# Performance work log

Measured on AMD Instinct MI355X. Metric: run time of the kernel, lower is better.

Reference implementation:

```python
import jax, jax.numpy as jnp
import numpy as np

N = 8192       # node_num
F_IN = 256     # src_feature
F_OUT = 128    # out_feature
NEG_SLOPE = 0.2  # standard GAT leakyrelu slope
MASK_VAL = -1e12


def setup_inputs() -> dict:
    key = jax.random.key(0)
    k1, k2, k3, k4, k5, k6 = jax.random.split(key, 6)
    x = jax.random.normal(k1, (N, F_IN), dtype=jnp.float32)
    adj = jax.random.randint(k2, (N, N), 0, 2, dtype=jnp.int32)  # 0/1 adjacency mask
    # xavier-uniform-like scales
    W = jax.random.normal(k3, (F_IN, F_OUT), dtype=jnp.float32) * np.float32(1.0 / np.sqrt(F_IN))
    a1 = jax.random.normal(k4, (F_OUT,), dtype=jnp.float32) * np.float32(0.1)  # att[:F_OUT]
    a2 = jax.random.normal(k5, (F_OUT,), dtype=jnp.float32) * np.float32(0.1)  # att[F_OUT:]
    bias = jax.random.normal(k6, (F_OUT,), dtype=jnp.float32) * np.float32(0.1)
    return {"x": x, "adj": adj, "W": W, "a1": a1, "a2": a2, "bias": bias}


def reference(x, adj, W, a1, a2, bias):
    # h = x @ W1  (src_h == dst_h for int src_dst_feature)
    h = x @ W  # [N, F_OUT]
    # e[i,j] = leakyrelu(att^T [h_i || h_j]) decomposed as (h@a1)_i + (h@a2)_j
    s_src = h @ a1  # [N]
    s_dst = h @ a2  # [N]
    e = jax.nn.leaky_relu(s_src[:, None] + s_dst[None, :], NEG_SLOPE)  # [N, N]
    masked = jnp.where(adj > 0, e, jnp.float32(MASK_VAL))
    attention = jax.nn.softmax(masked, axis=1)  # [N, N]
    # dropout in eval mode = identity; aggregate neighbor features
    out = attention @ h + bias  # [N, F_OUT]
    return out
```

## Files before the change

kernel.cpp:

```cpp
#include <hip/hip_runtime.h>
#include <cstdint>
#include <cstddef>

#define NN 8192
#define FIN 256
#define FOUT 128
#define SLOPE 0.2f
#define SHIFT 8.0f

typedef float f32x4 __attribute__((ext_vector_type(4)));
typedef __bf16 bf16x8 __attribute__((ext_vector_type(8)));
typedef int i32x4 __attribute__((ext_vector_type(4)));
typedef unsigned int u32x4 __attribute__((ext_vector_type(4)));

__device__ __forceinline__ unsigned short f2bf(float f) {
  return __builtin_bit_cast(unsigned short, (__bf16)f);
}

__device__ __forceinline__ void async_cp16(void* lds, const void* g) {
  __builtin_amdgcn_global_load_lds(
      (const __attribute__((address_space(1))) void*)g,
      (__attribute__((address_space(3))) void*)lds, 16, 0, 0);
}

__global__ __launch_bounds__(256, 4) void k_hw(const float* __restrict__ x,
                                               const float* __restrict__ W,
                                               const float* __restrict__ a1,
                                               const float* __restrict__ a2,
                                               unsigned short* __restrict__ ht,
                                               float* __restrict__ Etab,
                                               unsigned short* __restrict__ FbfF,
                                               unsigned short* __restrict__ FbfF2) {
  __shared__ float xs[8][256];
  __shared__ unsigned short tile[128][8];
  const int tid = threadIdx.x;
  const int rowbase = blockIdx.x * 8;

  #pragma unroll
  for (int it = 0; it < 2; ++it) {
    int fi = it * 1024 + tid * 4;
    int r = fi >> 8, k = fi & 255;
    *(f32x4*)&xs[r][k] = *(const f32x4*)(x + (size_t)(rowbase + r) * FIN + k);
  }
  __syncthreads();

  const int r = tid >> 5;
  const int cg = tid & 31;
  f32x4 acc = {0.f, 0.f, 0.f, 0.f};

  #pragma unroll 8
  for (int k = 0; k < FIN; ++k) {
    f32x4 wv = *(const f32x4*)(W + k * FOUT + cg * 4);
    float xv = xs[r][k];
    acc[0] += xv * wv[0];
    acc[1] += xv * wv[1];
    acc[2] += xv * wv[2];
    acc[3] += xv * wv[3];
  }

  #pragma unroll
  for (int c = 0; c < 4; ++c) tile[cg * 4 + c][r] = f2bf(acc[c]);

  f32x4 av1 = *(const f32x4*)(a1 + cg * 4);
  f32x4 av2 = *(const f32x4*)(a2 + cg * 4);
  float s1 = acc[0] * av1[0] + acc[1] * av1[1] + acc[2] * av1[2] + acc[3] * av1[3];
  float s2 = acc[0] * av2[0] + acc[1] * av2[1] + acc[2] * av2[2] + acc[3] * av2[3];
  #pragma unroll
  for (int off = 16; off > 0; off >>= 1) {
    s1 += __shfl_xor(s1, off, 64);
    s2 += __shfl_xor(s2, off, 64);
  }
  if (cg == 0) {
    const int row = rowbase + r;
    float c0 = s1 + SHIFT;
    float c = fmaxf(c0, SLOPE * c0);
    Etab[(size_t)row * 2]     = __expf(s1 - c);
    Etab[(size_t)row * 2 + 1] = __expf(SLOPE * s1 - c);
    FbfF[row]  = f2bf(__expf(s2));
    FbfF2[row] = f2bf(__expf(SLOPE * s2));
  }
  __syncthreads();

  if (tid < 128) {
    u32x4 v = *(const u32x4*)&tile[tid][0];
    *(u32x4*)(ht + (size_t)tid * NN + rowbase) = v;
  }
}

__global__ __launch_bounds__(256, 2) void k_gat(const int* __restrict__ adj,
                                                const unsigned short* __restrict__ ht,
                                                const float* __restrict__ Etab,
                                                const unsigned short* __restrict__ FbfF,
                                                const unsigned short* __restrict__ FbfF2,
                                                const float* __restrict__ bias,
                                                float* __restrict__ out) {
  __shared__ int sA[2][16 * 64];
  __shared__ unsigned short sH[2][128 * 64];
  __shared__ unsigned short sF[2][128];

  const int tid = threadIdx.x;
  const int wave = tid >> 6;
  const int lane = tid & 63;
  const int quad = lane >> 4;
  const int m = lane & 15;
  const int rowbase = blockIdx.x * 16;
  const int row = rowbase + m;

  bf16x8 pm, pinv, pones;
  #pragma unroll
  for (int jj = 0; jj < 8; ++jj) {
    pm[jj] = (__bf16)(float)m;
    pinv[jj] = (__bf16)0.03125f;
    pones[jj] = (__bf16)1.0f;
  }
  f32x4 z = {0.f, 0.f, 0.f, 0.f};
  f32x4 rp = __builtin_amdgcn_mfma_f32_16x16x32_bf16(pm, pinv, z, 0, 0, 0);
  f32x4 cp = __builtin_amdgcn_mfma_f32_16x16x32_bf16(pinv, pm, z, 0, 0, 0);
  int rowmap[4], colmap[4];
  #pragma unroll
  for (int r = 0; r < 4; ++r) {
    rowmap[r] = ((int)(rp[r] + 0.5f)) & 15;
    colmap[r] = ((int)(cp[r] + 0.5f)) & 15;
  }

  const float E  = Etab[(size_t)row * 2];
  const float E2 = Etab[(size_t)row * 2 + 1];

  const int t0 = wave * 2, t1 = wave * 2 + 1;

  f32x4 acc0 = z, acc1 = z, den = z;

  const unsigned short* srcH[4];
  #pragma unroll
  for (int il = 0; il < 4; ++il) {
    const int i = wave * 4 + il;
    const int f = i * 8 + (lane >> 3);
    const int g = (lane & 7) ^ (lane >> 3);
    srcH[il] = ht + (size_t)f * NN + g * 8;
  }
  const int* srcA[2] = {nullptr, nullptr};
  int slotA[2] = {0, 0};
  if (wave >= 2) {
    #pragma unroll
    for (int q = 0; q < 2; ++q) {
      const int il = (wave - 2) * 2 + q;
      const int r = il * 4 + (lane >> 4);
      const int g = (lane & 15) ^ r;
      slotA[q] = il;
      srcA[q] = adj + (size_t)(rowbase + r) * NN + g * 4;
    }
  }
  const unsigned short* srcF = nullptr;
  if (wave == 1) {
    srcF = (lane < 8) ? (FbfF + lane * 8) : (FbfF2 + (lane - 8) * 8);
  }

  auto stage = [&](int b) {
    #pragma unroll
    for (int il = 0; il < 4; ++il) {
      async_cp16(&sH[b][(wave * 4 + il) * 512], srcH[il]);
      srcH[il] += 64;
    }
    if (wave >= 2) {
      #pragma unroll
      for (int q = 0; q < 2; ++q) {
        async_cp16(&sA[b][slotA[q] * 256], srcA[q]);
        srcA[q] += 64;
      }
    } else if (wave == 1 && lane < 16) {
      async_cp16(&sF[b][0], srcF);
      srcF += 64;
    }
  };

  stage(0);

  for (int c = 0; c < 128; ++c) {
    const int cs = c & 1, ns = cs ^ 1;

    __syncthreads();
    if (c + 1 < 128) stage(ns);

    #pragma unroll
    for (int k32 = 0; k32 < 2; ++k32) {
      const int g0 = k32 * 8 + quad * 2;
      i32x4 A0 = *(const i32x4*)&sA[cs][m * 64 + ((g0) ^ m) * 4];
      i32x4 A1 = *(const i32x4*)&sA[cs][m * 64 + ((g0 + 1) ^ m) * 4];
      const int jl = k32 * 32 + quad * 8;
      u32x4 Fq = *(const u32x4*)&sF[cs][jl];
      u32x4 Gq = *(const u32x4*)&sF[cs][64 + jl];

      bf16x8 af;
      #pragma unroll
      for (int p = 0; p < 4; ++p) {
        const unsigned fp = Fq[p], gp = Gq[p];
        const float Flo = __builtin_bit_cast(float, fp << 16);
        const float Fhi = __builtin_bit_cast(float, fp & 0xffff0000u);
        const float Glo = __builtin_bit_cast(float, gp << 16);
        const float Ghi = __builtin_bit_cast(float, gp & 0xffff0000u);
        const float wlo = fmaxf(E * Flo, E2 * Glo);
        const float whi = fmaxf(E * Fhi, E2 * Ghi);
        const int avlo = (p < 2) ? A0[p * 2] : A1[p * 2 - 4];
        const int avhi = (p < 2) ? A0[p * 2 + 1] : A1[p * 2 - 3];
        af[p * 2]     = avlo ? (__bf16)wlo : (__bf16)0.0f;
        af[p * 2 + 1] = avhi ? (__bf16)whi : (__bf16)0.0f;
      }

      const int s0 = (k32 * 4 + quad) ^ (m & 7);
      bf16x8 b0 = __builtin_bit_cast(bf16x8,
          *(const u32x4*)&sH[cs][(t0 * 16 + m) * 64 + s0 * 8]);
      bf16x8 b1 = __builtin_bit_cast(bf16x8,
          *(const u32x4*)&sH[cs][(t1 * 16 + m) * 64 + s0 * 8]);

      acc0 = __builtin_amdgcn_mfma_f32_16x16x32_bf16(af, b0, acc0, 0, 0, 0);
      acc1 = __builtin_amdgcn_mfma_f32_16x16x32_bf16(af, b1, acc1, 0, 0, 0);
      den  = __builtin_amdgcn_mfma_f32_16x16x32_bf16(af, pones, den, 0, 0, 0);
    }
  }

  #pragma unroll
  for (int r = 0; r < 4; ++r) {
    const float inv = 1.0f / den[r];
    const int orow = rowbase + rowmap[r];
    const int c0 = t0 * 16 + colmap[r];
    const int c1 = t1 * 16 + colmap[r];
    out[(size_t)orow * FOUT + c0] = acc0[r] * inv + bias[c0];
    out[(size_t)orow * FOUT + c1] = acc1[r] * inv + bias[c1];
  }
}

extern "C" void kernel_launch(void* const* d_in, const int* in_sizes, int n_in,
                              void* d_out, int out_size, void* d_ws, size_t ws_size,
                              hipStream_t stream) {
  const float* x    = (const float*)d_in[0];
  const int*   adj  = (const int*)d_in[1];
  const float* W    = (const float*)d_in[2];
  const float* a1   = (const float*)d_in[3];
  const float* a2   = (const float*)d_in[4];
  const float* bias = (const float*)d_in[5];
  float* out = (float*)d_out;

  char* ws = (char*)d_ws;
  unsigned short* ht = (unsigned short*)ws;
  float* Etab = (float*)(ws + (size_t)2 * 1024 * 1024);
  unsigned short* FbfF =
      (unsigned short*)(ws + (size_t)2 * 1024 * 1024 + 64 * 1024);
  unsigned short* FbfF2 = FbfF + NN;

  k_hw<<<NN / 8, 256, 0, stream>>>(x, W, a1, a2, ht, Etab, FbfF, FbfF2);
  k_gat<<<NN / 16, 256, 0, stream>>>(adj, ht, Etab, FbfF, FbfF2, bias, out);
}
```

Baseline: 478.1 us.

## Pack adjacency into bitmask and replace LDS staging with direct register prefetch

Adds a pre-pass kernel that compresses the int32 adjacency matrix into a 1-bit-per-entry mask using wave ballots. The main GAT kernel then reads these mask words and the bf16 feature tiles straight from global memory into registers, prefetching one chunk ahead, instead of double-buffering through LDS with barriers. The 256 MB adjacency still has to be read once by the pack kernel, so the main cost is unchanged in volume. Dropping LDS and syncthreads removes shared traffic and barrier stalls. In exchange, the ht rows are re-read by every block from global/L2 without LDS sharing across waves, and an extra kernel launch is added.

```diff
diff --git a/kernel.cpp b/kernel.cpp
--- a/kernel.cpp
+++ b/kernel.cpp
@@ -10,17 +10,31 @@
 
 typedef float f32x4 __attribute__((ext_vector_type(4)));
 typedef __bf16 bf16x8 __attribute__((ext_vector_type(8)));
-typedef int i32x4 __attribute__((ext_vector_type(4)));
 typedef unsigned int u32x4 __attribute__((ext_vector_type(4)));
 
 __device__ __forceinline__ unsigned short f2bf(float f) {
   return __builtin_bit_cast(unsigned short, (__bf16)f);
 }
 
-__device__ __forceinline__ void async_cp16(void* lds, const void* g) {
-  __builtin_amdgcn_global_load_lds(
-      (const __attribute__((address_space(1))) void*)g,
-      (__attribute__((address_space(3))) void*)lds, 16, 0, 0);
+__global__ __launch_bounds__(256) void k_pack(const int* __restrict__ adj,
+                                              unsigned long long* __restrict__ mask) {
+  const int wid = blockIdx.x * 4 + (threadIdx.x >> 6);
+  const int lane = threadIdx.x & 63;
+  for (int s = wid; s < (NN * NN / 256); s += 8192) {
+    const int* base = adj + (size_t)s * 256;
+    int v0 = base[lane];
+    int v1 = base[lane + 64];
+    int v2 = base[lane + 128];
+    int v3 = base[lane + 192];
+    unsigned long long b0 = __ballot(v0 != 0);
+    unsigned long long b1 = __ballot(v1 != 0);
+    unsigned long long b2 = __ballot(v2 != 0);
+    unsigned long long b3 = __ballot(v3 != 0);
+    if (lane == 0) {
+      unsigned long long* q = mask + (size_t)s * 4;
+      q[0] = b0; q[1] = b1; q[2] = b2; q[3] = b3;
+    }
+  }
 }
 
 __global__ __launch_bounds__(256, 4) void k_hw(const float* __restrict__ x,
@@ -87,17 +101,13 @@
   }
 }
 
-__global__ __launch_bounds__(256, 2) void k_gat(const int* __restrict__ adj,
+__global__ __launch_bounds__(256, 2) void k_gat(const unsigned long long* __restrict__ mask,
                                                 const unsigned short* __restrict__ ht,
                                                 const float* __restrict__ Etab,
                                                 const unsigned short* __restrict__ FbfF,
                                                 const unsigned short* __restrict__ FbfF2,
                                                 const float* __restrict__ bias,
                                                 float* __restrict__ out) {
-  __shared__ int sA[2][16 * 64];
-  __shared__ unsigned short sH[2][128 * 64];
-  __shared__ unsigned short sF[2][128];
-
   const int tid = threadIdx.x;
   const int wave = tid >> 6;
   const int lane = tid & 63;
@@ -125,70 +135,49 @@
 
   const float E  = Etab[(size_t)row * 2];
   const float E2 = Etab[(size_t)row * 2 + 1];
-
   const int t0 = wave * 2, t1 = wave * 2 + 1;
 
+  const unsigned long long* mp = mask + (size_t)row * 128;
+  const unsigned short* fF = FbfF + quad * 8;
+  const unsigned short* fG = FbfF2 + quad * 8;
+  const unsigned short* hb0 = ht + (size_t)(t0 * 16 + m) * NN + quad * 8;
+  const unsigned short* hb1 = ht + (size_t)(t1 * 16 + m) * NN + quad * 8;
+
   f32x4 acc0 = z, acc1 = z, den = z;
 
-  const unsigned short* srcH[4];
-  #pragma unroll
-  for (int il = 0; il < 4; ++il) {
-    const int i = wave * 4 + il;
-    const int f = i * 8 + (lane >> 3);
-    const int g = (lane & 7) ^ (lane >> 3);
-    srcH[il] = ht + (size_t)f * NN + g * 8;
-  }
-  const int* srcA[2] = {nullptr, nullptr};
-  int slotA[2] = {0, 0};
-  if (wave >= 2) {
-    #pragma unroll
-    for (int q = 0; q < 2; ++q) {
-      const int il = (wave - 2) * 2 + q;
-      const int r = il * 4 + (lane >> 4);
-      const int g = (lane & 15) ^ r;
-      slotA[q] = il;
-      srcA[q] = adj + (size_t)(rowbase + r) * NN + g * 4;
-    }
-  }
-  const unsigned short* srcF = nullptr;
-  if (wave == 1) {
-    srcF = (lane < 8) ? (FbfF + lane * 8) : (FbfF2 + (lane - 8) * 8);
-  }
-
-  auto stage = [&](int b) {
-    #pragma unroll
-    for (int il = 0; il < 4; ++il) {
-      async_cp16(&sH[b][(wave * 4 + il) * 512], srcH[il]);
-      srcH[il] += 64;
-    }
-    if (wave >= 2) {
-      #pragma unroll
-      for (int q = 0; q < 2; ++q) {
-        async_cp16(&sA[b][slotA[q] * 256], srcA[q]);
-        srcA[q] += 64;
-      }
-    } else if (wave == 1 && lane < 16) {
-      async_cp16(&sF[b][0], srcF);
-      srcF += 64;
-    }
-  };
-
-  stage(0);
-
+  unsigned long long mk_n = mp[0];
+  u32x4 F0_n = *(const u32x4*)(fF);
+  u32x4 F1_n = *(const u32x4*)(fF + 32);
+  u32x4 G0_n = *(const u32x4*)(fG);
+  u32x4 G1_n = *(const u32x4*)(fG + 32);
+  u32x4 B00_n = *(const u32x4*)(hb0);
+  u32x4 B01_n = *(const u32x4*)(hb0 + 32);
+  u32x4 B10_n = *(const u32x4*)(hb1);
+  u32x4 B11_n = *(const u32x4*)(hb1 + 32);
+
+  #pragma unroll 1
   for (int c = 0; c < 128; ++c) {
-    const int cs = c & 1, ns = cs ^ 1;
-
-    __syncthreads();
-    if (c + 1 < 128) stage(ns);
+    unsigned long long mk = mk_n;
+    u32x4 F0 = F0_n, F1 = F1_n, G0 = G0_n, G1 = G1_n;
+    u32x4 B00 = B00_n, B01 = B01_n, B10 = B10_n, B11 = B11_n;
+
+    const int cn = (c + 1 < 128) ? (c + 1) : 127;
+    const int o = cn * 64;
+    mk_n = mp[cn];
+    F0_n = *(const u32x4*)(fF + o);
+    F1_n = *(const u32x4*)(fF + o + 32);
+    G0_n = *(const u32x4*)(fG + o);
+    G1_n = *(const u32x4*)(fG + o + 32);
+    B00_n = *(const u32x4*)(hb0 + o);
+    B01_n = *(const u32x4*)(hb0 + o + 32);
+    B10_n = *(const u32x4*)(hb1 + o);
+    B11_n = *(const u32x4*)(hb1 + o + 32);
 
     #pragma unroll
     for (int k32 = 0; k32 < 2; ++k32) {
-      const int g0 = k32 * 8 + quad * 2;
-      i32x4 A0 = *(const i32x4*)&sA[cs][m * 64 + ((g0) ^ m) * 4];
-      i32x4 A1 = *(const i32x4*)&sA[cs][m * 64 + ((g0 + 1) ^ m) * 4];
-      const int jl = k32 * 32 + quad * 8;
-      u32x4 Fq = *(const u32x4*)&sF[cs][jl];
-      u32x4 Gq = *(const u32x4*)&sF[cs][64 + jl];
+      const unsigned mb = (unsigned)(mk >> (k32 * 32 + quad * 8)) & 0xffu;
+      const u32x4 Fq = k32 ? F1 : F0;
+      const u32x4 Gq = k32 ? G1 : G0;
 
       bf16x8 af;
       #pragma unroll
@@ -200,18 +189,12 @@
         const float Ghi = __builtin_bit_cast(float, gp & 0xffff0000u);
         const float wlo = fmaxf(E * Flo, E2 * Glo);
         const float whi = fmaxf(E * Fhi, E2 * Ghi);
-        const int avlo = (p < 2) ? A0[p * 2] : A1[p * 2 - 4];
-        const int avhi = (p < 2) ? A0[p * 2 + 1] : A1[p * 2 - 3];
-        af[p * 2]     = avlo ? (__bf16)wlo : (__bf16)0.0f;
-        af[p * 2 + 1] = avhi ? (__bf16)whi : (__bf16)0.0f;
+        af[2 * p]     = ((mb >> (2 * p)) & 1u)     ? (__bf16)wlo : (__bf16)0.0f;
+        af[2 * p + 1] = ((mb >> (2 * p + 1)) & 1u) ? (__bf16)whi : (__bf16)0.0f;
       }
 
-      const int s0 = (k32 * 4 + quad) ^ (m & 7);
-      bf16x8 b0 = __builtin_bit_cast(bf16x8,
-          *(const u32x4*)&sH[cs][(t0 * 16 + m) * 64 + s0 * 8]);
-      bf16x8 b1 = __builtin_bit_cast(bf16x8,
-          *(const u32x4*)&sH[cs][(t1 * 16 + m) * 64 + s0 * 8]);
-
+      const bf16x8 b0 = __builtin_bit_cast(bf16x8, k32 ? B01 : B00);
+      const bf16x8 b1 = __builtin_bit_cast(bf16x8, k32 ? B11 : B10);
       acc0 = __builtin_amdgcn_mfma_f32_16x16x32_bf16(af, b0, acc0, 0, 0, 0);
       acc1 = __builtin_amdgcn_mfma_f32_16x16x32_bf16(af, b1, acc1, 0, 0, 0);
       den  = __builtin_amdgcn_mfma_f32_16x16x32_bf16(af, pones, den, 0, 0, 0);
@@ -241,12 +224,14 @@
   float* out = (float*)d_out;
 
   char* ws = (char*)d_ws;
-  unsigned short* ht = (unsigned short*)ws;
-  float* Etab = (float*)(ws + (size_t)2 * 1024 * 1024);
+  unsigned long long* maskq = (unsigned long long*)ws;
+  unsigned short* ht = (unsigned short*)(ws + (size_t)8 * 1024 * 1024);
+  float* Etab = (float*)(ws + (size_t)10 * 1024 * 1024);
   unsigned short* FbfF =
-      (unsigned short*)(ws + (size_t)2 * 1024 * 1024 + 64 * 1024);
+      (unsigned short*)(ws + (size_t)10 * 1024 * 1024 + 64 * 1024);
   unsigned short* FbfF2 = FbfF + NN;
 
+  k_pack<<<2048, 256, 0, stream>>>(adj, maskq);
   k_hw<<<NN / 8, 256, 0, stream>>>(x, W, a1, a2, ht, Etab, FbfF, FbfF2);
-  k_gat<<<NN / 16, 256, 0, stream>>>(adj, ht, Etab, FbfF, FbfF2, bias, out);
-}
+  k_gat<<<NN / 16, 256, 0, stream>>>(maskq, ht, Etab, FbfF, FbfF2, bias, out);
+}
```

Result: slower. 621.8 us (+30.1%).
